# Optimization experiments

Measured on AMD Instinct MI355X. Metric: run time of the kernel, lower is better.

The kernel has to match this reference:

```python
import jax, jax.numpy as jnp
import numpy as np

B = 32          # graphs per batch
NPG = 2048      # nodes per graph
N = B * NPG     # 65536 total nodes
EPG = 16384     # edges per graph
E = B * EPG     # 524288 total edges
F_IN = 129
H, C = 4, 64    # heads, per-head channels
HC = H * C      # 256
NEG_SLOPE = 0.2 # GATConv LeakyReLU slope


def setup_inputs() -> dict:
    key = jax.random.key(0)
    ks = jax.random.split(key, 20)
    # node features
    x = jax.random.normal(ks[0], (N, F_IN), dtype=jnp.float32)
    # random edges, endpoints within the same graph (per-graph contiguous node ids)
    off = (jnp.arange(B) * NPG)[:, None]
    src = (jax.random.randint(ks[1], (B, EPG), 0, NPG) + off).reshape(-1)
    dst = (jax.random.randint(ks[2], (B, EPG), 0, NPG) + off).reshape(-1)
    edge_index = jnp.stack([src, dst]).astype(jnp.int64)

    def lin(k, fan_in, shape):
        return jax.random.normal(k, shape, dtype=jnp.float32) / np.sqrt(fan_in)

    return {
        "x": x,
        "edge_index": edge_index,
        "lin0_w": lin(ks[3], F_IN, (F_IN, 256)),
        "lin0_b": jnp.zeros((256,), jnp.float32),
        "gat0_W": lin(ks[4], 256, (256, HC)),
        "gat0_asrc": lin(ks[5], C, (H, C)),
        "gat0_adst": lin(ks[6], C, (H, C)),
        "gat0_b": jnp.zeros((HC,), jnp.float32),
        "pool0_w": lin(ks[7], HC, (HC,)),
        "gat1_W": lin(ks[8], HC, (HC, HC)),
        "gat1_asrc": lin(ks[9], C, (H, C)),
        "gat1_adst": lin(ks[10], C, (H, C)),
        "gat1_b": jnp.zeros((HC,), jnp.float32),
        "pool1_w": lin(ks[11], HC, (HC,)),
        "gate_w": lin(ks[12], HC, (HC, 1)),
        "gate_b": jnp.zeros((1,), jnp.float32),
    }


def _leaky(z):
    return jnp.where(z > 0, z, NEG_SLOPE * z)


def _gat(h_in, src, dst, emask, W, asrc, adst, b):
    """PyG GATConv: shared lin, edge attention, segment softmax over dest, self-loops, concat heads."""
    n = h_in.shape[0]
    h = (h_in @ W).reshape(n, H, C)                       # [n,H,C]
    loops = jnp.arange(n)
    s = jnp.concatenate([src, loops])                     # add self loops
    d = jnp.concatenate([dst, loops])
    m = jnp.concatenate([emask, jnp.ones((n,), bool)])
    a_s = jnp.einsum('nhc,hc->nh', h, asrc)               # [n,H]
    a_d = jnp.einsum('nhc,hc->nh', h, adst)
    logit = _leaky(a_s[s] + a_d[d])                       # [E+n,H]
    logit = jnp.where(m[:, None], logit, -1e9)
    mx = jax.ops.segment_max(logit, d, num_segments=n)    # stable segment softmax
    ex = jnp.exp(logit - mx[d]) * m[:, None].astype(logit.dtype)
    den = jax.ops.segment_sum(ex, d, num_segments=n)
    coef = ex / (den[d] + 1e-16)                          # [E+n,H]
    out = jax.ops.segment_sum(h[s] * coef[:, :, None], d, num_segments=n)
    return out.reshape(n, HC) + b


def _topk_pool(hx, src, dst, emask, w, n_in, k):
    """PyG TopKPooling: score = x.w/||w||, per-graph top-k, x' = x[perm]*tanh(score[perm]), edge filter+reindex."""
    n_tot = hx.shape[0]
    bb = n_tot // n_in
    score = (hx @ w) / (jnp.linalg.norm(w) + 1e-16)       # [n_tot]
    _, idx = jax.lax.top_k(score.reshape(bb, n_in), k)    # [bb,k]
    perm = (idx + (jnp.arange(bb) * n_in)[:, None]).reshape(-1)
    xs = hx[perm] * jnp.tanh(score[perm])[:, None]
    newid = jnp.full((n_tot,), -1, jnp.int32).at[perm].set(jnp.arange(bb * k, dtype=jnp.int32))
    ns, nd = newid[src], newid[dst]
    valid = emask & (ns >= 0) & (nd >= 0)
    ns = jnp.where(valid, ns, 0)
    nd = jnp.where(valid, nd, 0)
    return xs, ns, nd, valid


def _attpool(hx, n, gate_w, gate_b):
    """AttentionalAggregation: softmax(gate_nn(x)) per graph, weighted sum."""
    bb = hx.shape[0] // n
    gate = (hx @ gate_w + gate_b).reshape(bb, n)
    wts = jax.nn.softmax(gate, axis=1)
    return jnp.einsum('bn,bnf->bf', wts, hx.reshape(bb, n, -1))


def reference(x, edge_index, lin0_w, lin0_b, gat0_W, gat0_asrc, gat0_adst, gat0_b,
              pool0_w, gat1_W, gat1_asrc, gat1_adst, gat1_b, pool1_w, gate_w, gate_b):
    src, dst = edge_index[0], edge_index[1]
    emask = jnp.ones((E,), bool)
    h = jax.nn.relu(x @ lin0_w + lin0_b)                                  # hidden MLP
    h = jax.nn.elu(_gat(h, src, dst, emask, gat0_W, gat0_asrc, gat0_adst, gat0_b))
    h, src, dst, emask = _topk_pool(h, src, dst, emask, pool0_w, NPG, NPG // 2)
    out = _attpool(h, NPG // 2, gate_w, gate_b)                           # [B,256]
    h = jax.nn.elu(_gat(h, src, dst, emask, gat1_W, gat1_asrc, gat1_adst, gat1_b))
    h, src, dst, emask = _topk_pool(h, src, dst, emask, pool1_w, NPG // 2, NPG // 4)
    out = out + _attpool(h, NPG // 4, gate_w, gate_b)
    return out
```

## Files before the change

kernel.cpp:

```cpp
#include <hip/hip_runtime.h>
#include <cmath>

namespace {

constexpr int NN0 = 65536;
constexpr int NB  = 32;
constexpr int NE  = 524288;
constexpr int EPG = 16384;
constexpr int FIN = 129;
constexpr int KP  = 160;

typedef short bf16x8 __attribute__((ext_vector_type(8)));
typedef float f32x4 __attribute__((ext_vector_type(4)));

__device__ inline float leakyrelu(float z) { return z > 0.f ? z : 0.2f * z; }
__device__ inline float eluf(float z) { return z > 0.f ? z : expm1f(z); }

__device__ inline unsigned short f2bf(float x) {
  union { float f; unsigned int u; } v; v.f = x;
  unsigned int r = v.u + 0x7fffu + ((v.u >> 16) & 1u);
  return (unsigned short)(r >> 16);
}
__device__ inline float bf2f(unsigned short h) {
  union { unsigned int u; float f; } v; v.u = ((unsigned int)h) << 16;
  return v.f;
}

__device__ inline float4 f4fma(float4 a, float c, float4 acc) {
  acc.x += a.x * c; acc.y += a.y * c; acc.z += a.z * c; acc.w += a.w * c;
  return acc;
}

__device__ inline int swz_block(int bid, int bpgl) {
  int x = bid & 7;
  int local = bid >> 3;
  int g = x + ((local >> bpgl) << 3);
  return (g << bpgl) + (local & ((1 << bpgl) - 1));
}

__device__ __forceinline__ void gload_lds16(const unsigned short* g, unsigned short* l) {
  __builtin_amdgcn_global_load_lds((const unsigned int*)g, (unsigned int*)l, 16, 0, 0);
}

__device__ inline void pack_w_body(const float* __restrict__ W, int Kreal, int idx,
                                   unsigned short* __restrict__ hi,
                                   unsigned short* __restrict__ lo) {
  int j = idx & 7;
  int lane = (idx >> 3) & 63;
  int ct = (idx >> 9) & 15;
  int kt = idx >> 13;
  int k = kt * 32 + ((lane >> 4) << 3) + j;
  int c = ct * 16 + (lane & 15);
  float v = (k < Kreal) ? W[(size_t)k * 256 + c] : 0.f;
  unsigned short h = f2bf(v);
  hi[idx] = h;
  lo[idx] = f2bf(v - bf2f(h));
}

__global__ void prep(const float* __restrict__ x,
                     const float* __restrict__ w0, const float* __restrict__ w1,
                     const float* __restrict__ w2,
                     const float* __restrict__ pw0, const float* __restrict__ pw1,
                     unsigned short* __restrict__ xhi, unsigned short* __restrict__ xlo,
                     unsigned short* __restrict__ whi0, unsigned short* __restrict__ wlo0,
                     unsigned short* __restrict__ whi1, unsigned short* __restrict__ wlo1,
                     unsigned short* __restrict__ whi2, unsigned short* __restrict__ wlo2,
                     float* __restrict__ norms, int* __restrict__ newid) {
  const int NX = NN0 * KP / 256;
  const int NW0 = 5 * 8192 / 256;
  const int NW = 8 * 8192 / 256;
  const int NC = NN0 / 256;
  int b = blockIdx.x, tid = threadIdx.x;
  if (b < NX) {
    int idx = b * 256 + tid;
    int row = idx / KP, c = idx - row * KP;
    float v = (c < FIN) ? x[(size_t)row * FIN + c] : 0.f;
    unsigned short h = f2bf(v);
    xhi[idx] = h;
    xlo[idx] = f2bf(v - bf2f(h));
    return;
  }
  b -= NX;
  if (b < NW0) { pack_w_body(w0, FIN, b * 256 + tid, whi0, wlo0); return; }
  b -= NW0;
  if (b < NW) { pack_w_body(w1, 256, b * 256 + tid, whi1, wlo1); return; }
  b -= NW;
  if (b < NW) { pack_w_body(w2, 256, b * 256 + tid, whi2, wlo2); return; }
  b -= NW;
  if (b < NC) {
    newid[b * 256 + tid] = -1;
    return;
  }
  if (tid < 64) {
    float a0 = 0.f, a1 = 0.f;
#pragma unroll
    for (int j = tid; j < 256; j += 64) {
      float v0 = pw0[j]; a0 += v0 * v0;
      float v1 = pw1[j]; a1 += v1 * v1;
    }
#pragma unroll
    for (int off = 32; off >= 1; off >>= 1) {
      a0 += __shfl_xor(a0, off);
      a1 += __shfl_xor(a1, off);
    }
    if (tid == 0) {
      norms[0] = 1.f / (sqrtf(a0) + 1e-16f);
      norms[1] = 1.f / (sqrtf(a1) + 1e-16f);
    }
  }
}

__global__ __launch_bounds__(256, 2) void gemm_fused(
    const unsigned short* __restrict__ Xhi, const unsigned short* __restrict__ Xlo,
    const unsigned short* __restrict__ B0hi, const unsigned short* __restrict__ B0lo,
    const float* __restrict__ bias0,
    const unsigned short* __restrict__ B1hi, const unsigned short* __restrict__ B1lo,
    float* __restrict__ Out,
    const float* __restrict__ attsrc, const float* __restrict__ attdst,
    float* __restrict__ a_s, float* __restrict__ a_d) {
  __shared__ __align__(16) unsigned short As[2][2][64][32];
  __shared__ __align__(16) char Hsh[2][64 * 512];
  const int tid = threadIdx.x;
  const int lane = tid & 63;
  const int w = tid >> 6;
  const int row0 = blockIdx.x * 64;
  const int l15 = lane & 15, q = lane >> 4;
  const int srow16 = lane >> 2;
  const int skc = (lane & 3) * 8;

  auto stage = [&](int nb, int kt) {
    const size_t goff = (size_t)(row0 + w * 16 + srow16) * KP + kt * 32 + skc;
    gload_lds16(Xhi + goff, &As[nb][0][w * 16][0]);
    gload_lds16(Xlo + goff, &As[nb][1][w * 16][0]);
  };

  f32x4 acc[4][4];
#pragma unroll
  for (int mf = 0; mf < 4; mf++)
#pragma unroll
    for (int nf = 0; nf < 4; nf++) acc[mf][nf] = (f32x4)(0.f);

  stage(0, 0);
  __syncthreads();

#pragma unroll
  for (int kt = 0; kt < 5; ++kt) {
    const int nb = kt & 1;
    if (kt + 1 < 5) stage(nb ^ 1, kt + 1);
    bf16x8 bh[4], bl[4];
#pragma unroll
    for (int nf = 0; nf < 4; nf++) {
      const int ct = w * 4 + nf;
      const size_t bbase = ((size_t)((kt * 16 + ct) * 64 + lane)) << 3;
      bh[nf] = *reinterpret_cast<const bf16x8*>(B0hi + bbase);
      bl[nf] = *reinterpret_cast<const bf16x8*>(B0lo + bbase);
    }
#pragma unroll
    for (int mf = 0; mf < 4; mf++) {
      const int ar = mf * 16 + l15;
      bf16x8 ah = *reinterpret_cast<const bf16x8*>(&As[nb][0][ar][q * 8]);
      bf16x8 al = *reinterpret_cast<const bf16x8*>(&As[nb][1][ar][q * 8]);
#pragma unroll
      for (int nf = 0; nf < 4; nf++) {
        acc[mf][nf] = __builtin_amdgcn_mfma_f32_16x16x32_bf16(ah, bh[nf], acc[mf][nf], 0, 0, 0);
        acc[mf][nf] = __builtin_amdgcn_mfma_f32_16x16x32_bf16(ah, bl[nf], acc[mf][nf], 0, 0, 0);
        acc[mf][nf] = __builtin_amdgcn_mfma_f32_16x16x32_bf16(al, bh[nf], acc[mf][nf], 0, 0, 0);
      }
    }
    __syncthreads();
  }

#pragma unroll
  for (int mf = 0; mf < 4; mf++) {
#pragma unroll
    for (int r = 0; r < 4; r++) {
      const int row = mf * 16 + q * 4 + r;
#pragma unroll
      for (int nf = 0; nf < 4; nf++) {
        const int col = w * 64 + nf * 16 + l15;
        float v = acc[mf][nf][r] + bias0[col];
        v = fmaxf(v, 0.f);
        unsigned short h = f2bf(v);
        unsigned short l = f2bf(v - bf2f(h));
        unsigned int off = (unsigned int)(row * 512 + col * 2) ^ ((row & 7) << 4);
        *reinterpret_cast<unsigned short*>(&Hsh[0][off]) = h;
        *reinterpret_cast<unsigned short*>(&Hsh[1][off]) = l;
        acc[mf][nf][r] = 0.f;
      }
    }
  }
  __syncthreads();

#pragma unroll
  for (int kt = 0; kt < 8; ++kt) {
    bf16x8 bh[4], bl[4];
#pragma unroll
    for (int nf = 0; nf < 4; nf++) {
      const int ct = w * 4 + nf;
      const size_t bbase = ((size_t)((kt * 16 + ct) * 64 + lane)) << 3;
      bh[nf] = *reinterpret_cast<const bf16x8*>(B1hi + bbase);
      bl[nf] = *reinterpret_cast<const bf16x8*>(B1lo + bbase);
    }
#pragma unroll
    for (int mf = 0; mf < 4; mf++) {
      const int ar = mf * 16 + l15;
      unsigned int off = (unsigned int)(ar * 512 + kt * 64 + q * 16) ^ ((ar & 7) << 4);
      bf16x8 ah = *reinterpret_cast<const bf16x8*>(&Hsh[0][off]);
      bf16x8 al = *reinterpret_cast<const bf16x8*>(&Hsh[1][off]);
#pragma unroll
      for (int nf = 0; nf < 4; nf++) {
        acc[mf][nf] = __builtin_amdgcn_mfma_f32_16x16x32_bf16(ah, bh[nf], acc[mf][nf], 0, 0, 0);
        acc[mf][nf] = __builtin_amdgcn_mfma_f32_16x16x32_bf16(ah, bl[nf], acc[mf][nf], 0, 0, 0);
        acc[mf][nf] = __builtin_amdgcn_mfma_f32_16x16x32_bf16(al, bh[nf], acc[mf][nf], 0, 0, 0);
      }
    }
  }

#pragma unroll
  for (int mf = 0; mf < 4; mf++) {
    const int rowb = row0 + mf * 16 + q * 4;
#pragma unroll
    for (int r = 0; r < 4; r++) {
#pragma unroll
      for (int nf = 0; nf < 4; nf++) {
        const int col = w * 64 + nf * 16 + l15;
        Out[(size_t)(rowb + r) * 256 + col] = acc[mf][nf][r];
      }
    }
  }
  const int head = w;
  float sv[4], dv[4];
#pragma unroll
  for (int nf = 0; nf < 4; nf++) {
    sv[nf] = attsrc[head * 64 + nf * 16 + l15];
    dv[nf] = attdst[head * 64 + nf * 16 + l15];
  }
#pragma unroll
  for (int mf = 0; mf < 4; mf++) {
#pragma unroll
    for (int r = 0; r < 4; r++) {
      float ps = 0.f, pd = 0.f;
#pragma unroll
      for (int nf = 0; nf < 4; nf++) {
        ps += acc[mf][nf][r] * sv[nf];
        pd += acc[mf][nf][r] * dv[nf];
      }
#pragma unroll
      for (int off = 8; off >= 1; off >>= 1) {
        ps += __shfl_xor(ps, off);
        pd += __shfl_xor(pd, off);
      }
      if (l15 == 0) {
        const int row = row0 + mf * 16 + q * 4 + r;
        a_s[(size_t)row * 4 + head] = ps;
        a_d[(size_t)row * 4 + head] = pd;
      }
    }
  }
}

template <int KT, bool INDIR>
__global__ __launch_bounds__(256, 2) void gemm_mfma(
    const unsigned short* __restrict__ Xhi, const unsigned short* __restrict__ Xlo,
    int ldx,
    const unsigned short* __restrict__ Bhi, const unsigned short* __restrict__ Blo,
    float* __restrict__ Out,
    const float* __restrict__ attsrc, const float* __restrict__ attdst,
    float* __restrict__ a_s, float* __restrict__ a_d,
    const int* __restrict__ rowmap, const float* __restrict__ tscale, int swzl) {
  __shared__ __align__(16) unsigned short As[2][2][128][32];
  const int tid = threadIdx.x;
  const int lane = tid & 63;
  const int w = tid >> 6;
  const int rb = (swzl >= 0) ? swz_block(blockIdx.x, swzl) : blockIdx.x;
  const int row0 = rb * 128;
  const int l15 = lane & 15, q = lane >> 4;
  const int sl4 = lane >> 2;
  const int skc = (lane & 3) * 8;

  size_t gr[2];
#pragma unroll
  for (int i = 0; i < 2; i++) {
    int lr = row0 + (w + 4 * i) * 16 + sl4;
    gr[i] = INDIR ? (size_t)rowmap[lr] : (size_t)lr;
  }

  auto stage = [&](int nb, int kt) {
#pragma unroll
    for (int i = 0; i < 2; i++) {
      const int rbase = (w + 4 * i) * 16;
      const size_t goff = gr[i] * ldx + kt * 32 + skc;
      gload_lds16(Xhi + goff, &As[nb][0][rbase][0]);
      gload_lds16(Xlo + goff, &As[nb][1][rbase][0]);
    }
  };

  f32x4 acc[8][4];
#pragma unroll
  for (int mf = 0; mf < 8; mf++)
#pragma unroll
    for (int nf = 0; nf < 4; nf++) acc[mf][nf] = (f32x4)(0.f);

  stage(0, 0);
  __syncthreads();

#pragma unroll
  for (int kt = 0; kt < KT; ++kt) {
    const int nb = kt & 1;
    if (kt + 1 < KT) stage(nb ^ 1, kt + 1);
    bf16x8 bh[4], bl[4];
#pragma unroll
    for (int nf = 0; nf < 4; nf++) {
      const int ct = w * 4 + nf;
      const size_t bbase = ((size_t)((kt * 16 + ct) * 64 + lane)) << 3;
      bh[nf] = *reinterpret_cast<const bf16x8*>(Bhi + bbase);
      bl[nf] = *reinterpret_cast<const bf16x8*>(Blo + bbase);
    }
#pragma unroll
    for (int mf = 0; mf < 8; mf++) {
      const int ar = mf * 16 + l15;
      bf16x8 ah = *reinterpret_cast<const bf16x8*>(&As[nb][0][ar][q * 8]);
      bf16x8 al = *reinterpret_cast<const bf16x8*>(&As[nb][1][ar][q * 8]);
#pragma unroll
      for (int nf = 0; nf < 4; nf++) {
        acc[mf][nf] = __builtin_amdgcn_mfma_f32_16x16x32_bf16(ah, bh[nf], acc[mf][nf], 0, 0, 0);
        acc[mf][nf] = __builtin_amdgcn_mfma_f32_16x16x32_bf16(ah, bl[nf], acc[mf][nf], 0, 0, 0);
        acc[mf][nf] = __builtin_amdgcn_mfma_f32_16x16x32_bf16(al, bh[nf], acc[mf][nf], 0, 0, 0);
      }
    }
    __syncthreads();
  }

#pragma unroll
  for (int mf = 0; mf < 8; mf++) {
    const int rowb = row0 + mf * 16 + q * 4;
#pragma unroll
    for (int r = 0; r < 4; r++) {
      const float ts = INDIR ? tscale[rowb + r] : 1.f;
#pragma unroll
      for (int nf = 0; nf < 4; nf++) {
        float v = acc[mf][nf][r];
        if constexpr (INDIR) v *= ts;
        const int col = w * 64 + nf * 16 + l15;
        Out[(size_t)(rowb + r) * 256 + col] = v;
      }
    }
  }
  const int head = w;
  float sv[4], dv[4];
#pragma unroll
  for (int nf = 0; nf < 4; nf++) {
    sv[nf] = attsrc[head * 64 + nf * 16 + l15];
    dv[nf] = attdst[head * 64 + nf * 16 + l15];
  }
#pragma unroll
  for (int mf = 0; mf < 8; mf++) {
#pragma unroll
    for (int r = 0; r < 4; r++) {
      float ps = 0.f, pd = 0.f;
#pragma unroll
      for (int nf = 0; nf < 4; nf++) {
        ps += acc[mf][nf][r] * sv[nf];
        pd += acc[mf][nf][r] * dv[nf];
      }
#pragma unroll
      for (int off = 8; off >= 1; off >>= 1) {
        ps += __shfl_xor(ps, off);
        pd += __shfl_xor(pd, off);
      }
      if (l15 == 0) {
        const int row = row0 + mf * 16 + q * 4 + r;
        float ts = INDIR ? tscale[row] : 1.f;
        a_s[(size_t)row * 4 + head] = ps * ts;
        a_d[(size_t)row * 4 + head] = pd * ts;
      }
    }
  }
}

__global__ __launch_bounds__(1024) void scatter0L(const int* __restrict__ src,
                                                  const int* __restrict__ dst,
                                                  int* __restrict__ cursor,
                                                  int* __restrict__ csr) {
  __shared__ int cnt[2048];
  const int g = blockIdx.x, tid = threadIdx.x;
  cnt[tid] = 0;
  cnt[tid + 1024] = 0;
  __syncthreads();
  const int e0 = g * EPG;
  for (int i = tid; i < EPG; i += 1024) {
    int e = e0 + i;
    int d = dst[e];
    int pos = atomicAdd(&cnt[d - (g << 11)], 1);
    if (pos < 64) csr[(size_t)d * 64 + pos] = src[e];
  }
  __syncthreads();
  cursor[(g << 11) + tid] = cnt[tid];
  cursor[(g << 11) + tid + 1024] = cnt[tid + 1024];
}

__global__ __launch_bounds__(1024) void scatter1L(const int* __restrict__ src,
                                                  const int* __restrict__ dst,
                                                  const int* __restrict__ newid,
                                                  int* __restrict__ cursor,
                                                  int* __restrict__ csr) {
  __shared__ int cnt[1024];
  const int g = blockIdx.x, tid = threadIdx.x;
  cnt[tid] = 0;
  __syncthreads();
  const int e0 = g * EPG;
  for (int i = tid; i < EPG; i += 1024) {
    int e = e0 + i;
    int s = newid[src[e]], d = newid[dst[e]];
    if (s < 0 || d < 0) continue;
    int pos = atomicAdd(&cnt[d - (g << 10)], 1);
    if (pos < 64) csr[(size_t)d * 64 + pos] = s;
  }
  __syncthreads();
  cursor[(g << 10) + tid] = cnt[tid];
}

__global__ __launch_bounds__(256) void gat_node8(
    const int* __restrict__ cursor, const int* __restrict__ csr,
    const float* __restrict__ a_s, const float* __restrict__ a_d,
    const float* __restrict__ hW, const float* __restrict__ bias,
    const float* __restrict__ pool_w, const float* __restrict__ inv_norm,
    const float* __restrict__ gate_w,
    unsigned short* __restrict__ outHi, unsigned short* __restrict__ outLo,
    float* __restrict__ score, float* __restrict__ graw, int bpgl) {
  const int lane = threadIdx.x & 63;
  const int wv = threadIdx.x >> 6;
  const int dbase = swz_block(blockIdx.x, bpgl) * 8 + wv * 2;
  const int g = lane >> 4, l16 = lane & 15;
  const int d = dbase + (g >> 1);
  const int h0 = (g & 1) * 2;

  const int deg = min(cursor[d], 63);
  const int dim = deg + 1;

  int dmaxw = dim;
  dmaxw = max(dmaxw, __shfl_xor(dmaxw, 32));
  const int nch = (dmaxw + 15) >> 4;

  const float2 ad2 = *reinterpret_cast<const float2*>(&a_d[(size_t)d * 4 + h0]);

  int sreg[4];
  float L0[4], L1[4];
#pragma unroll
  for (int c = 0; c < 4; c++) {
    if (c < nch) {
      const int j = c * 16 + l16;
      const bool has = j < dim;
      int s = (j < deg) ? csr[(size_t)d * 64 + j] : d;
      sreg[c] = s;
      float2 as2 = *reinterpret_cast<const float2*>(&a_s[(size_t)s * 4 + h0]);
      L0[c] = has ? leakyrelu(as2.x + ad2.x) : -1e30f;
      L1[c] = has ? leakyrelu(as2.y + ad2.y) : -1e30f;
    } else {
      sreg[c] = d;
      L0[c] = -1e30f; L1[c] = -1e30f;
    }
  }
  float m0 = fmaxf(fmaxf(L0[0], L0[1]), fmaxf(L0[2], L0[3]));
  float m1 = fmaxf(fmaxf(L1[0], L1[1]), fmaxf(L1[2], L1[3]));
#pragma unroll
  for (int off = 1; off <= 8; off <<= 1) {
    m0 = fmaxf(m0, __shfl_xor(m0, off));
    m1 = fmaxf(m1, __shfl_xor(m1, off));
  }
  float e0[4], e1[4];
  float dn0 = 0.f, dn1 = 0.f;
#pragma unroll
  for (int c = 0; c < 4; c++) {
    if (c < nch) {
      e0[c] = __expf(L0[c] - m0);
      e1[c] = __expf(L1[c] - m1);
      dn0 += e0[c]; dn1 += e1[c];
    } else {
      e0[c] = 0.f; e1[c] = 0.f;
    }
  }
#pragma unroll
  for (int off = 1; off <= 8; off <<= 1) {
    dn0 += __shfl_xor(dn0, off);
    dn1 += __shfl_xor(dn1, off);
  }

  float4 acc0 = {0.f, 0.f, 0.f, 0.f}, acc1 = {0.f, 0.f, 0.f, 0.f};
#pragma unroll
  for (int c = 0; c < 4; c++) {
    if (c < nch) {
      const int tmax = min(16, dmaxw - c * 16);
#pragma unroll 2
      for (int tt = 0; tt < tmax; tt++) {
        const int idx = g * 16 + tt;
        int st = __shfl(sreg[c], idx);
        float c0 = __shfl(e0[c], idx), c1 = __shfl(e1[c], idx);
        if (c * 16 + tt < dim) {
          const float4* hp = reinterpret_cast<const float4*>(&hW[(size_t)st * 256]) + l16;
          acc0 = f4fma(hp[h0 * 16],       c0, acc0);
          acc1 = f4fma(hp[(h0 + 1) * 16], c1, acc1);
        }
      }
    }
  }

  const float iv0 = 1.f / (dn0 + 1e-16f), iv1 = 1.f / (dn1 + 1e-16f);
  float sd = 0.f, gd = 0.f;
#pragma unroll
  for (int h = 0; h < 2; h++) {
    const int coff = (h0 + h) * 64 + l16 * 4;
    float4 vb = h ? acc1 : acc0;
    float iv = h ? iv1 : iv0;
    float4 bb = *reinterpret_cast<const float4*>(&bias[coff]);
    float4 o;
    o.x = eluf(vb.x * iv + bb.x);
    o.y = eluf(vb.y * iv + bb.y);
    o.z = eluf(vb.z * iv + bb.z);
    o.w = eluf(vb.w * iv + bb.w);
    ushort4 oh, ol;
    oh.x = f2bf(o.x); ol.x = f2bf(o.x - bf2f(oh.x));
    oh.y = f2bf(o.y); ol.y = f2bf(o.y - bf2f(oh.y));
    oh.z = f2bf(o.z); ol.z = f2bf(o.z - bf2f(oh.z));
    oh.w = f2bf(o.w); ol.w = f2bf(o.w - bf2f(oh.w));
    *reinterpret_cast<ushort4*>(&outHi[(size_t)d * 256 + coff]) = oh;
    *reinterpret_cast<ushort4*>(&outLo[(size_t)d * 256 + coff]) = ol;
    float4 pw = *reinterpret_cast<const float4*>(&pool_w[coff]);
    float4 gw = *reinterpret_cast<const float4*>(&gate_w[coff]);
    sd += o.x * pw.x + o.y * pw.y + o.z * pw.z + o.w * pw.w;
    gd += o.x * gw.x + o.y * gw.y + o.z * gw.z + o.w * gw.w;
  }
#pragma unroll
  for (int off = 1; off <= 16; off <<= 1) {
    sd += __shfl_xor(sd, off);
    gd += __shfl_xor(gd, off);
  }
  if ((lane & 31) == 0) {
    score[d] = sd * inv_norm[0];
    graw[d] = gd;
  }
}

__global__ __launch_bounds__(1024) void topk_hsel(
    const float* __restrict__ score, const float* __restrict__ graw,
    const float* __restrict__ gate_b, int npg, int k,
    int* __restrict__ perm, int* __restrict__ newid,
    float* __restrict__ gate, float* __restrict__ tsc) {
  __shared__ unsigned keys[2048];
  __shared__ int hist[1024];
  __shared__ int ssum[1024];
  __shared__ int segtot[16];
  __shared__ unsigned wmin[16], wmax[16];
  __shared__ int sstate[3];
  __shared__ int scnt;
  __shared__ int candi[512];
  __shared__ unsigned candk[512];
  __shared__ float fred[1024];
  const int g = blockIdx.x, tid = threadIdx.x;
  const int wv = tid >> 6, ln = tid & 63;
  const size_t base = (size_t)g * npg;

  unsigned mymin = 0xFFFFFFFFu, mymax = 0u;
  for (int i = tid; i < npg; i += 1024) {
    unsigned u = __float_as_uint(score[base + i]);
    u = (u & 0x80000000u) ? ~u : (u | 0x80000000u);
    keys[i] = u;
    mymin = min(mymin, u);
    mymax = max(mymax, u);
  }
#pragma unroll
  for (int off = 32; off >= 1; off >>= 1) {
    mymin = min(mymin, (unsigned)__shfl_xor((int)mymin, off));
    mymax = max(mymax, (unsigned)__shfl_xor((int)mymax, off));
  }
  if (ln == 0) { wmin[wv] = mymin; wmax[wv] = mymax; }
  __syncthreads();
  unsigned lo, hi;
  {
    unsigned a = 0xFFFFFFFFu, b = 0u;
#pragma unroll
    for (int i = 0; i < 16; i++) { a = min(a, wmin[i]); b = max(b, wmax[i]); }
    lo = a; hi = b;
  }
  int need = k;

  for (int iter = 0; iter < 4; ++iter) {
    unsigned long long range = (unsigned long long)(hi - lo) + 1ull;
    unsigned width = (unsigned)((range + 1023ull) >> 10);
    hist[tid] = 0;
    __syncthreads();
    for (int i = tid; i < npg; i += 1024) {
      unsigned u = keys[i];
      if (u >= lo && u <= hi) atomicAdd(&hist[(u - lo) / width], 1);
    }
    __syncthreads();
    int v = hist[tid];
    int s = v;
#pragma unroll
    for (int off = 1; off < 64; off <<= 1) {
      int t = __shfl_down(s, off);
      if (ln + off < 64) s += t;
    }
    if (ln == 0) segtot[wv] = s;
    __syncthreads();
    if (tid == 0) {
      int acc = 0;
      for (int i = 15; i >= 0; i--) { int t = segtot[i]; segtot[i] = acc; acc += t; }
    }
    __syncthreads();
    int S = s + segtot[wv];
    ssum[tid] = S;
    __syncthreads();
    int gt = (tid == 1023) ? 0 : ssum[tid + 1];
    if (S >= need && gt < need) {
      sstate[0] = tid;
      sstate[1] = gt;
      sstate[2] = hist[tid];
    }
    __syncthreads();
    const int bstar = sstate[0], cntAbove = sstate[1], m = sstate[2];
    unsigned nlo = lo + (unsigned)bstar * width;
    unsigned long long nhiu = (unsigned long long)lo + (unsigned long long)(bstar + 1) * width - 1ull;
    unsigned nhi = (nhiu > (unsigned long long)hi) ? hi : (unsigned)nhiu;
    need -= cntAbove;
    lo = nlo; hi = nhi;
    __syncthreads();
    if (width == 1 || m <= 256) break;
  }

  if (tid == 0) scnt = 0;
  __syncthreads();
  for (int i = tid; i < npg; i += 1024) {
    unsigned u = keys[i];
    if (u >= lo && u <= hi) {
      int pidx = atomicAdd(&scnt, 1);
      if (pidx < 512) { candi[pidx] = i; candk[pidx] = u; }
    }
  }
  __syncthreads();
  const int m_all = scnt;
  const float gb = gate_b[0];
  if (tid == 0) scnt = 0;
  __syncthreads();
  for (int i = tid; i < npg; i += 1024) {
    if (keys[i] > hi) {
      int pos = atomicAdd(&scnt, 1);
      int node = (int)(base + i);
      perm[g * k + pos] = node;
      if (newid) newid[node] = g * k + pos;
      float ts = tanhf(score[base + i]);
      tsc[g * k + pos] = ts;
      gate[g * k + pos] = ts * graw[node] + gb;
    }
  }
  __syncthreads();
  const int nAbove = scnt;
  if (m_all <= 512) {
    for (int c = tid; c < m_all; c += 1024) {
      unsigned u = candk[c];
      int i = candi[c];
      int rank = 0;
      for (int j = 0; j < m_all; j++) {
        unsigned vk = candk[j];
        rank += (vk > u) || (vk == u && candi[j] < i);
      }
      if (rank < need) {
        int pos = nAbove + rank;
        int node = (int)(base + i);
        perm[g * k + pos] = node;
        if (newid) newid[node] = g * k + pos;
        float ts = tanhf(score[base + i]);
        tsc[g * k + pos] = ts;
        gate[g * k + pos] = ts * graw[node] + gb;
      }
    }
  } else {
    for (int i = tid; i < npg; i += 1024) {
      unsigned u = keys[i];
      if (u >= lo && u <= hi) {
        int rank = 0;
        for (int j = 0; j < npg; j++) {
          unsigned vk = keys[j];
          if (vk >= lo && vk <= hi) rank += (vk > u) || (vk == u && j < i);
        }
        if (rank < need) {
          int pos = nAbove + rank;
          int node = (int)(base + i);
          perm[g * k + pos] = node;
          if (newid) newid[node] = g * k + pos;
          float ts = tanhf(score[base + i]);
          tsc[g * k + pos] = ts;
          gate[g * k + pos] = ts * graw[node] + gb;
        }
      }
    }
  }
  __syncthreads();

  float gv = (tid < k) ? gate[g * k + tid] : -1e30f;
  fred[tid] = gv;
  __syncthreads();
  for (int s = 512; s >= 1; s >>= 1) {
    if (tid < s) fred[tid] = fmaxf(fred[tid], fred[tid + s]);
    __syncthreads();
  }
  const float gm = fred[0];
  __syncthreads();
  float ge = (tid < k) ? __expf(gv - gm) : 0.f;
  fred[tid] = ge;
  __syncthreads();
  for (int s = 512; s >= 1; s >>= 1) {
    if (tid < s) fred[tid] += fred[tid + s];
    __syncthreads();
  }
  const float ginv = 1.f / fred[0];
  if (tid < k) gate[g * k + tid] = ge * ginv * tsc[g * k + tid];
}

__global__ __launch_bounds__(256) void attpool_sum(const unsigned short* __restrict__ xhi,
                                                   const unsigned short* __restrict__ xlo,
                                                   const int* __restrict__ perm,
                                                   const float* __restrict__ wfin,
                                                   float* __restrict__ partials,
                                                   int npg, int bpgl) {
  int o = swz_block(blockIdx.x, bpgl);
  int g = o >> bpgl, sub = o & ((1 << bpgl) - 1);
  size_t r0 = (size_t)g * npg + sub * 32;
  int c = threadIdx.x;
  float a = 0.f;
#pragma unroll 8
  for (int i = 0; i < 32; i++) {
    float wv = wfin[r0 + i];
    size_t node = (size_t)perm[r0 + i];
    float v = bf2f(xhi[node * 256 + c]) + bf2f(xlo[node * 256 + c]);
    a += wv * v;
  }
  partials[(size_t)o * 256 + c] = a;
}

__global__ __launch_bounds__(256) void attpool_reduce(const float* __restrict__ partials,
                                                      float* __restrict__ out,
                                                      int nch, int acc_flag) {
  int g = blockIdx.x, c = threadIdx.x;
  float a = 0.f;
  for (int s = 0; s < nch; s++) a += partials[((size_t)g * nch + s) * 256 + c];
  if (acc_flag) out[g * 256 + c] += a;
  else out[g * 256 + c] = a;
}

}

extern "C" void kernel_launch(void* const* d_in, const int* in_sizes, int n_in,
                              void* d_out, int out_size, void* d_ws, size_t ws_size,
                              hipStream_t stream) {
  (void)in_sizes; (void)n_in; (void)out_size; (void)ws_size;
  const float* x       = (const float*)d_in[0];
  const int*   ei      = (const int*)d_in[1];
  const float* lin0_w  = (const float*)d_in[2];
  const float* lin0_b  = (const float*)d_in[3];
  const float* gat0_W  = (const float*)d_in[4];
  const float* gat0_as = (const float*)d_in[5];
  const float* gat0_ad = (const float*)d_in[6];
  const float* gat0_b  = (const float*)d_in[7];
  const float* pool0_w = (const float*)d_in[8];
  const float* gat1_W  = (const float*)d_in[9];
  const float* gat1_as = (const float*)d_in[10];
  const float* gat1_ad = (const float*)d_in[11];
  const float* gat1_b  = (const float*)d_in[12];
  const float* pool1_w = (const float*)d_in[13];
  const float* gate_w  = (const float*)d_in[14];
  const float* gate_b  = (const float*)d_in[15];
  float* out = (float*)d_out;
  const int* srcp = ei;
  const int* dstp = ei + NE;

  char* wsb = (char*)d_ws;
  size_t cur = 0;
  auto alloc = [&](size_t bytes) {
    void* p = wsb + cur;
    cur = (cur + bytes + 255) & ~(size_t)255;
    return p;
  };
  char* regA = (char*)alloc((size_t)NN0 * 256 * 4);
  char* regB = (char*)alloc((size_t)NN0 * 256 * 4);
  char* regD = (char*)alloc((size_t)NN0 * KP * 2 * 2);
  float* a_s     = (float*)alloc((size_t)NN0 * 4 * 4);
  float* a_d     = (float*)alloc((size_t)NN0 * 4 * 4);
  int*   cursor  = (int*)alloc((size_t)NN0 * 4);
  int*   cursor2 = (int*)alloc((size_t)32768 * 4);
  int*   csr     = (int*)alloc((size_t)NN0 * 64 * 4);
  float* score   = (float*)alloc((size_t)NN0 * 4);
  float* graw    = (float*)alloc((size_t)NN0 * 4);
  int*   newid   = (int*)alloc((size_t)NN0 * 4);
  int*   perm0   = (int*)alloc((size_t)32768 * 4);
  int*   perm1   = (int*)alloc((size_t)16384 * 4);
  float* tsc0    = (float*)alloc((size_t)32768 * 4);
  float* tsc1    = (float*)alloc((size_t)16384 * 4);
  float* gate0   = (float*)alloc((size_t)32768 * 4);
  float* gate1   = (float*)alloc((size_t)16384 * 4);
  float* partials= (float*)alloc((size_t)NB * 32 * 256 * 4);
  float* norms   = (float*)alloc(2 * 4);
  unsigned short* whi0 = (unsigned short*)alloc((size_t)5 * 8192 * 2);
  unsigned short* wlo0 = (unsigned short*)alloc((size_t)5 * 8192 * 2);
  unsigned short* whi1 = (unsigned short*)alloc((size_t)8 * 8192 * 2);
  unsigned short* wlo1 = (unsigned short*)alloc((size_t)8 * 8192 * 2);
  unsigned short* whi2 = (unsigned short*)alloc((size_t)8 * 8192 * 2);
  unsigned short* wlo2 = (unsigned short*)alloc((size_t)8 * 8192 * 2);

  unsigned short* xhi = (unsigned short*)regD;
  unsigned short* xlo = xhi + (size_t)NN0 * KP;
  float* hW0  = (float*)regB;
  unsigned short* out0hi = (unsigned short*)regA;
  unsigned short* out0lo = out0hi + (size_t)NN0 * 256;
  float* hW1  = (float*)regB;
  unsigned short* out1hi = (unsigned short*)(regB + (size_t)32768 * 256 * 4);
  unsigned short* out1lo = out1hi + (size_t)32768 * 256;

  {
    int grid = NN0 * KP / 256 + 160 + 256 + 256 + 256 + 1;
    prep<<<grid, 256, 0, stream>>>(x, lin0_w, gat0_W, gat1_W, pool0_w, pool1_w,
                                   xhi, xlo, whi0, wlo0, whi1, wlo1, whi2, wlo2,
                                   norms, newid);
  }

  scatter0L<<<NB, 1024, 0, stream>>>(srcp, dstp, cursor, csr);

  gemm_fused<<<NN0 / 64, 256, 0, stream>>>(
      xhi, xlo, whi0, wlo0, lin0_b, whi1, wlo1, hW0,
      gat0_as, gat0_ad, a_s, a_d);

  gat_node8<<<NN0 / 8, 256, 0, stream>>>(cursor, csr, a_s, a_d, hW0,
                                         gat0_b, pool0_w, norms, gate_w,
                                         out0hi, out0lo, score, graw, 8);

  topk_hsel<<<NB, 1024, 0, stream>>>(score, graw, gate_b, 2048, 1024,
                                     perm0, newid, gate0, tsc0);
  attpool_sum<<<NB * 32, 256, 0, stream>>>(out0hi, out0lo, perm0, gate0,
                                           partials, 1024, 5);
  attpool_reduce<<<NB, 256, 0, stream>>>(partials, out, 32, 0);

  scatter1L<<<NB, 1024, 0, stream>>>(srcp, dstp, newid, cursor2, csr);
  gemm_mfma<8, true><<<32768 / 128, 256, 0, stream>>>(
      out0hi, out0lo, 256, whi2, wlo2, hW1,
      gat1_as, gat1_ad, a_s, a_d, perm0, tsc0, 3);
  gat_node8<<<32768 / 8, 256, 0, stream>>>(cursor2, csr, a_s, a_d, hW1,
                                           gat1_b, pool1_w, norms + 1, gate_w,
                                           out1hi, out1lo, score, graw, 7);

  topk_hsel<<<NB, 1024, 0, stream>>>(score, graw, gate_b, 1024, 512,
                                     perm1, nullptr, gate1, tsc1);
  attpool_sum<<<NB * 16, 256, 0, stream>>>(out1hi, out1lo, perm1, gate1,
                                           partials, 512, 4);
  attpool_reduce<<<NB, 256, 0, stream>>>(partials, out, 16, 1);
}
```

Before: 275.5 us.

## Merge small kernels into neighbouring launches to cut launch count

Folds the layer-0 edge scatter into the prep kernel, which now uses 1024-thread blocks. The attention-pool partial sums and the layer-1 scatter are merged into one pool_tail kernel, and the layer-0 attpool reduce is done by extra blocks appended to the layer-1 GEMM grid. This removes several launches and their gaps. In exchange, prep and pool_tail carry 2048- and 1024-int shared arrays in every block, which can cut occupancy for the elementwise blocks, and the merged kernels mix workloads of different shapes.

Result: faster. 263.6 us (-4.3%).

```diff
diff --git a/kernel.cpp b/kernel.cpp
--- a/kernel.cpp
+++ b/kernel.cpp
@@ -57,22 +57,26 @@
   lo[idx] = f2bf(v - bf2f(h));
 }
 
-__global__ void prep(const float* __restrict__ x,
-                     const float* __restrict__ w0, const float* __restrict__ w1,
-                     const float* __restrict__ w2,
-                     const float* __restrict__ pw0, const float* __restrict__ pw1,
-                     unsigned short* __restrict__ xhi, unsigned short* __restrict__ xlo,
-                     unsigned short* __restrict__ whi0, unsigned short* __restrict__ wlo0,
-                     unsigned short* __restrict__ whi1, unsigned short* __restrict__ wlo1,
-                     unsigned short* __restrict__ whi2, unsigned short* __restrict__ wlo2,
-                     float* __restrict__ norms, int* __restrict__ newid) {
-  const int NX = NN0 * KP / 256;
-  const int NW0 = 5 * 8192 / 256;
-  const int NW = 8 * 8192 / 256;
-  const int NC = NN0 / 256;
+__global__ __launch_bounds__(1024) void prep(
+    const float* __restrict__ x,
+    const float* __restrict__ w0, const float* __restrict__ w1,
+    const float* __restrict__ w2,
+    const float* __restrict__ pw0, const float* __restrict__ pw1,
+    const int* __restrict__ src, const int* __restrict__ dst,
+    unsigned short* __restrict__ xhi, unsigned short* __restrict__ xlo,
+    unsigned short* __restrict__ whi0, unsigned short* __restrict__ wlo0,
+    unsigned short* __restrict__ whi1, unsigned short* __restrict__ wlo1,
+    unsigned short* __restrict__ whi2, unsigned short* __restrict__ wlo2,
+    float* __restrict__ norms, int* __restrict__ newid,
+    int* __restrict__ cursor, int* __restrict__ csr) {
+  __shared__ int cnt[2048];
+  const int NX = NN0 * KP / 1024;
+  const int NW0 = 5 * 8192 / 1024;
+  const int NW = 8 * 8192 / 1024;
+  const int NC = NN0 / 1024;
   int b = blockIdx.x, tid = threadIdx.x;
   if (b < NX) {
-    int idx = b * 256 + tid;
+    int idx = b * 1024 + tid;
     int row = idx / KP, c = idx - row * KP;
     float v = (c < FIN) ? x[(size_t)row * FIN + c] : 0.f;
     unsigned short h = f2bf(v);
@@ -81,14 +85,32 @@
     return;
   }
   b -= NX;
-  if (b < NW0) { pack_w_body(w0, FIN, b * 256 + tid, whi0, wlo0); return; }
+  if (b < NW0) { pack_w_body(w0, FIN, b * 1024 + tid, whi0, wlo0); return; }
   b -= NW0;
-  if (b < NW) { pack_w_body(w1, 256, b * 256 + tid, whi1, wlo1); return; }
+  if (b < NW) { pack_w_body(w1, 256, b * 1024 + tid, whi1, wlo1); return; }
   b -= NW;
-  if (b < NW) { pack_w_body(w2, 256, b * 256 + tid, whi2, wlo2); return; }
+  if (b < NW) { pack_w_body(w2, 256, b * 1024 + tid, whi2, wlo2); return; }
   b -= NW;
   if (b < NC) {
-    newid[b * 256 + tid] = -1;
+    newid[b * 1024 + tid] = -1;
+    return;
+  }
+  b -= NC;
+  if (b < NB) {
+    const int g = b;
+    cnt[tid] = 0;
+    cnt[tid + 1024] = 0;
+    __syncthreads();
+    const int e0 = g * EPG;
+    for (int i = tid; i < EPG; i += 1024) {
+      int e = e0 + i;
+      int d = dst[e];
+      int pos = atomicAdd(&cnt[d - (g << 11)], 1);
+      if (pos < 64) csr[(size_t)d * 64 + pos] = src[e];
+    }
+    __syncthreads();
+    cursor[(g << 11) + tid] = cnt[tid];
+    cursor[(g << 11) + tid + 1024] = cnt[tid + 1024];
     return;
   }
   if (tid < 64) {
@@ -267,9 +289,18 @@
     float* __restrict__ Out,
     const float* __restrict__ attsrc, const float* __restrict__ attdst,
     float* __restrict__ a_s, float* __restrict__ a_d,
-    const int* __restrict__ rowmap, const float* __restrict__ tscale, int swzl) {
+    const int* __restrict__ rowmap, const float* __restrict__ tscale, int swzl,
+    int ngemm, const float* __restrict__ partials, float* __restrict__ outp,
+    int nch) {
   __shared__ __align__(16) unsigned short As[2][2][128][32];
   const int tid = threadIdx.x;
+  if ((int)blockIdx.x >= ngemm) {
+    int g = blockIdx.x - ngemm, c = tid;
+    float a = 0.f;
+    for (int s = 0; s < nch; s++) a += partials[((size_t)g * nch + s) * 256 + c];
+    outp[g * 256 + c] = a;
+    return;
+  }
   const int lane = tid & 63;
   const int w = tid >> 6;
   const int rb = (swzl >= 0) ? swz_block(blockIdx.x, swzl) : blockIdx.x;
@@ -376,48 +407,6 @@
       }
     }
   }
-}
-
-__global__ __launch_bounds__(1024) void scatter0L(const int* __restrict__ src,
-                                                  const int* __restrict__ dst,
-                                                  int* __restrict__ cursor,
-                                                  int* __restrict__ csr) {
-  __shared__ int cnt[2048];
-  const int g = blockIdx.x, tid = threadIdx.x;
-  cnt[tid] = 0;
-  cnt[tid + 1024] = 0;
-  __syncthreads();
-  const int e0 = g * EPG;
-  for (int i = tid; i < EPG; i += 1024) {
-    int e = e0 + i;
-    int d = dst[e];
-    int pos = atomicAdd(&cnt[d - (g << 11)], 1);
-    if (pos < 64) csr[(size_t)d * 64 + pos] = src[e];
-  }
-  __syncthreads();
-  cursor[(g << 11) + tid] = cnt[tid];
-  cursor[(g << 11) + tid + 1024] = cnt[tid + 1024];
-}
-
-__global__ __launch_bounds__(1024) void scatter1L(const int* __restrict__ src,
-                                                  const int* __restrict__ dst,
-                                                  const int* __restrict__ newid,
-                                                  int* __restrict__ cursor,
-                                                  int* __restrict__ csr) {
-  __shared__ int cnt[1024];
-  const int g = blockIdx.x, tid = threadIdx.x;
-  cnt[tid] = 0;
-  __syncthreads();
-  const int e0 = g * EPG;
-  for (int i = tid; i < EPG; i += 1024) {
-    int e = e0 + i;
-    int s = newid[src[e]], d = newid[dst[e]];
-    if (s < 0 || d < 0) continue;
-    int pos = atomicAdd(&cnt[d - (g << 10)], 1);
-    if (pos < 64) csr[(size_t)d * 64 + pos] = s;
-  }
-  __syncthreads();
-  cursor[(g << 10) + tid] = cnt[tid];
 }
 
 __global__ __launch_bounds__(256) void gat_node8(
@@ -717,25 +706,46 @@
   if (tid < k) gate[g * k + tid] = ge * ginv * tsc[g * k + tid];
 }
 
-__global__ __launch_bounds__(256) void attpool_sum(const unsigned short* __restrict__ xhi,
-                                                   const unsigned short* __restrict__ xlo,
-                                                   const int* __restrict__ perm,
-                                                   const float* __restrict__ wfin,
-                                                   float* __restrict__ partials,
-                                                   int npg, int bpgl) {
-  int o = swz_block(blockIdx.x, bpgl);
-  int g = o >> bpgl, sub = o & ((1 << bpgl) - 1);
-  size_t r0 = (size_t)g * npg + sub * 32;
-  int c = threadIdx.x;
-  float a = 0.f;
+__global__ __launch_bounds__(1024) void pool_tail(
+    const unsigned short* __restrict__ xhi, const unsigned short* __restrict__ xlo,
+    const int* __restrict__ perm, const float* __restrict__ wfin,
+    float* __restrict__ partials, int npg, int bpgl, int nsum,
+    const int* __restrict__ src, const int* __restrict__ dst,
+    const int* __restrict__ newid, int* __restrict__ cursor2,
+    int* __restrict__ csr, int do_scatter) {
+  __shared__ int cnt[1024];
+  const int tid = threadIdx.x;
+  if ((int)blockIdx.x < nsum) {
+    int o = swz_block(blockIdx.x, bpgl);
+    int g = o >> bpgl, lb = o & ((1 << bpgl) - 1);
+    int part = tid >> 8, c = tid & 255;
+    int sub = lb * 4 + part;
+    size_t r0 = (size_t)g * npg + sub * 32;
+    float a = 0.f;
 #pragma unroll 8
-  for (int i = 0; i < 32; i++) {
-    float wv = wfin[r0 + i];
-    size_t node = (size_t)perm[r0 + i];
-    float v = bf2f(xhi[node * 256 + c]) + bf2f(xlo[node * 256 + c]);
-    a += wv * v;
-  }
-  partials[(size_t)o * 256 + c] = a;
+    for (int i = 0; i < 32; i++) {
+      float wv = wfin[r0 + i];
+      size_t node = (size_t)perm[r0 + i];
+      float v = bf2f(xhi[node * 256 + c]) + bf2f(xlo[node * 256 + c]);
+      a += wv * v;
+    }
+    partials[((size_t)g * (npg >> 5) + sub) * 256 + c] = a;
+    return;
+  }
+  if (!do_scatter) return;
+  const int g = blockIdx.x - nsum;
+  cnt[tid] = 0;
+  __syncthreads();
+  const int e0 = g * EPG;
+  for (int i = tid; i < EPG; i += 1024) {
+    int e = e0 + i;
+    int s = newid[src[e]], d = newid[dst[e]];
+    if (s < 0 || d < 0) continue;
+    int pos = atomicAdd(&cnt[d - (g << 10)], 1);
+    if (pos < 64) csr[(size_t)d * 64 + pos] = s;
+  }
+  __syncthreads();
+  cursor2[(g << 10) + tid] = cnt[tid];
 }
 
 __global__ __launch_bounds__(256) void attpool_reduce(const float* __restrict__ partials,
@@ -817,13 +827,12 @@
   unsigned short* out1lo = out1hi + (size_t)32768 * 256;
 
   {
-    int grid = NN0 * KP / 256 + 160 + 256 + 256 + 256 + 1;
-    prep<<<grid, 256, 0, stream>>>(x, lin0_w, gat0_W, gat1_W, pool0_w, pool1_w,
-                                   xhi, xlo, whi0, wlo0, whi1, wlo1, whi2, wlo2,
-                                   norms, newid);
-  }
-
-  scatter0L<<<NB, 1024, 0, stream>>>(srcp, dstp, cursor, csr);
+    int grid = NN0 * KP / 1024 + 40 + 64 + 64 + 64 + NB + 1;
+    prep<<<grid, 1024, 0, stream>>>(x, lin0_w, gat0_W, gat1_W, pool0_w, pool1_w,
+                                    srcp, dstp,
+                                    xhi, xlo, whi0, wlo0, whi1, wlo1, whi2, wlo2,
+                                    norms, newid, cursor, csr);
+  }
 
   gemm_fused<<<NN0 / 64, 256, 0, stream>>>(
       xhi, xlo, whi0, wlo0, lin0_b, whi1, wlo1, hW0,
@@ -835,21 +844,24 @@
 
   topk_hsel<<<NB, 1024, 0, stream>>>(score, graw, gate_b, 2048, 1024,
                                      perm0, newid, gate0, tsc0);
-  attpool_sum<<<NB * 32, 256, 0, stream>>>(out0hi, out0lo, perm0, gate0,
-                                           partials, 1024, 5);
-  attpool_reduce<<<NB, 256, 0, stream>>>(partials, out, 32, 0);
-
-  scatter1L<<<NB, 1024, 0, stream>>>(srcp, dstp, newid, cursor2, csr);
-  gemm_mfma<8, true><<<32768 / 128, 256, 0, stream>>>(
+  pool_tail<<<NB * 8 + NB, 1024, 0, stream>>>(out0hi, out0lo, perm0, gate0,
+                                              partials, 1024, 3, NB * 8,
+                                              srcp, dstp, newid, cursor2, csr, 1);
+
+  gemm_mfma<8, true><<<32768 / 128 + NB, 256, 0, stream>>>(
       out0hi, out0lo, 256, whi2, wlo2, hW1,
-      gat1_as, gat1_ad, a_s, a_d, perm0, tsc0, 3);
+      gat1_as, gat1_ad, a_s, a_d, perm0, tsc0, 3,
+      32768 / 128, partials, out, 32);
+
   gat_node8<<<32768 / 8, 256, 0, stream>>>(cursor2, csr, a_s, a_d, hW1,
                                            gat1_b, pool1_w, norms + 1, gate_w,
                                            out1hi, out1lo, score, graw, 7);
 
   topk_hsel<<<NB, 1024, 0, stream>>>(score, graw, gate_b, 1024, 512,
                                      perm1, nullptr, gate1, tsc1);
-  attpool_sum<<<NB * 16, 256, 0, stream>>>(out1hi, out1lo, perm1, gate1,
-                                           partials, 512, 4);
+  pool_tail<<<NB * 4, 1024, 0, stream>>>(out1hi, out1lo, perm1, gate1,
+                                         partials, 512, 2, NB * 4,
+                                         nullptr, nullptr, nullptr, nullptr,
+                                         nullptr, 0);
   attpool_reduce<<<NB, 256, 0, stream>>>(partials, out, 16, 1);
 }
```
